# Kernel tuning notes

Hardware: AMD Instinct MI355X
Metric: run time of the kernel (lower is better)

## Reference

```python
import jax, jax.numpy as jnp
import numpy as np

DIM = 1024
DEPTH = 7
PAR = 8
N_NODES = 2 ** (DEPTH + 1) - 1  # 255
WIDTH = PAR * N_NODES  # 2040


def setup_inputs() -> dict:
    key = jax.random.key(0)
    k1, k2, k3, k4 = jax.random.split(key, 4)
    init_k = float(np.sqrt(1.0 / DIM))
    init_k2 = float(np.sqrt(1.0 / ((DEPTH + 1) * PAR)))
    oldx = jax.random.normal(k1, (4, 2048, DIM), dtype=jnp.float32)
    W_in = jax.random.uniform(k2, (WIDTH, DIM), jnp.float32, -init_k, init_k)
    b_in = jax.random.uniform(k3, (WIDTH,), jnp.float32, -init_k, init_k)
    W_out = jax.random.uniform(k4, (DIM, WIDTH), jnp.float32, -init_k2, init_k2)
    return {"oldx": oldx, "W_in": W_in, "b_in": b_in, "W_out": W_out}


def reference(oldx, W_in, b_in, W_out):
    x = oldx.reshape(-1, DIM)                      # [B, dim]
    B = x.shape[0]
    logits = x @ W_in.T + b_in                     # [B, width] dense GEMM over ALL nodes
    decisions = (logits > 0).astype(jnp.int32).reshape(B, PAR, N_NODES)
    acts = jax.nn.silu(logits).reshape(B, PAR, N_NODES)

    # Tree traversal: mark root, then descend DEPTH levels by each node's sign bit.
    current = jnp.zeros((B, PAR), dtype=jnp.int32)
    dmap = jax.nn.one_hot(current, N_NODES, dtype=acts.dtype)  # root node marked
    for d in range(DEPTH):
        cur_platform = 2 ** d - 1
        next_platform = 2 ** (d + 1) - 1
        moves = jnp.take_along_axis(decisions, current[..., None], axis=2)[..., 0]
        current = (current - cur_platform) * 2 + moves + next_platform
        dmap = dmap + jax.nn.one_hot(current, N_NODES, dtype=acts.dtype)

    masked = acts * jax.lax.stop_gradient(dmap)    # only depth+1 nodes per tree survive
    out = masked.reshape(B, WIDTH) @ W_out.T       # [B, dim]
    return out.reshape(oldx.shape)
```

## Files before the change

### kernel.cpp

```cpp
#include <hip/hip_runtime.h>
#include <math.h>

#define DIM 1024
#define DEPTH 7
#define PAR 8
#define N_NODES 255
#define WIDTH 2040
#define MARGIN 0.01f

#define REPLANE(p) ((((p) & 1) << 3) | ((((p) >> 1) & 1) << 4) | ((((p) >> 2) & 1) << 5))

typedef _Float16 half2v __attribute__((ext_vector_type(2)));

__device__ __forceinline__ half2v as_h2(unsigned int u) {
    union { unsigned int u; half2v h; } c; c.u = u; return c.h;
}
__device__ __forceinline__ unsigned int pack_h2(float a, float b) {
    union { half2v h; unsigned int u; } c;
    c.h = (half2v){(_Float16)a, (_Float16)b};
    return c.u;
}

__device__ __forceinline__ float dot2h(unsigned int a, unsigned int b, float c) {
#if __has_builtin(__builtin_amdgcn_fdot2)
    return __builtin_amdgcn_fdot2(as_h2(a), as_h2(b), c, false);
#else
    half2v ha = as_h2(a), hb = as_h2(b);
    c = fmaf((float)ha.x, (float)hb.x, c);
    return fmaf((float)ha.y, (float)hb.y, c);
#endif
}

__device__ __forceinline__ float foldK(float a, float b, int K) {
    const bool hi = (threadIdx.x & (unsigned)K) != 0;
    const float keep = hi ? b : a;
    const float send = hi ? a : b;
    return keep + __shfl_xor(send, K, 64);
}

#define PHASE_C_TREE(WLO, WHI, A) do {                                                      \
    const float a_ = (A); half2v h_;                                                        \
    h_ = as_h2((WLO).x); acc[0]  = fmaf((float)h_.x, a_, acc[0]);  acc[1]  = fmaf((float)h_.y, a_, acc[1]);  \
    h_ = as_h2((WLO).y); acc[2]  = fmaf((float)h_.x, a_, acc[2]);  acc[3]  = fmaf((float)h_.y, a_, acc[3]);  \
    h_ = as_h2((WLO).z); acc[4]  = fmaf((float)h_.x, a_, acc[4]);  acc[5]  = fmaf((float)h_.y, a_, acc[5]);  \
    h_ = as_h2((WLO).w); acc[6]  = fmaf((float)h_.x, a_, acc[6]);  acc[7]  = fmaf((float)h_.y, a_, acc[7]);  \
    h_ = as_h2((WHI).x); acc[8]  = fmaf((float)h_.x, a_, acc[8]);  acc[9]  = fmaf((float)h_.y, a_, acc[9]);  \
    h_ = as_h2((WHI).y); acc[10] = fmaf((float)h_.x, a_, acc[10]); acc[11] = fmaf((float)h_.y, a_, acc[11]); \
    h_ = as_h2((WHI).z); acc[12] = fmaf((float)h_.x, a_, acc[12]); acc[13] = fmaf((float)h_.y, a_, acc[13]); \
    h_ = as_h2((WHI).w); acc[14] = fmaf((float)h_.x, a_, acc[14]); acc[15] = fmaf((float)h_.y, a_, acc[15]); \
} while (0)

#define TRANS_BLOCKS 512

__global__ __launch_bounds__(256) void prep_kernel(
    const float* __restrict__ W_out,
    const float* __restrict__ W_in,
    unsigned short* __restrict__ WoT,
    unsigned int* __restrict__ Wh)
{
    __shared__ float tile[64][65];
    if (blockIdx.x < TRANS_BLOCKS) {
        const int w0 = (int)(blockIdx.x & 31) * 64;
        const int d0 = (int)(blockIdx.x >> 5) * 64;
        const int tid = (int)threadIdx.x;
        const int sub = tid & 15;
        const int grp = tid >> 4;

        #pragma unroll
        for (int pass = 0; pass < 4; ++pass) {
            const int dl = pass * 16 + grp;
            const int wl = sub * 4;
            const int w = w0 + wl;
            const int d = d0 + dl;
            float4 v = make_float4(0.f, 0.f, 0.f, 0.f);
            if (w + 3 < WIDTH) {
                v = *(const float4*)(W_out + (size_t)d * WIDTH + w);
            } else {
                float t0 = (w + 0 < WIDTH) ? W_out[(size_t)d * WIDTH + w + 0] : 0.f;
                float t1 = (w + 1 < WIDTH) ? W_out[(size_t)d * WIDTH + w + 1] : 0.f;
                float t2 = (w + 2 < WIDTH) ? W_out[(size_t)d * WIDTH + w + 2] : 0.f;
                float t3 = (w + 3 < WIDTH) ? W_out[(size_t)d * WIDTH + w + 3] : 0.f;
                v = make_float4(t0, t1, t2, t3);
            }
            tile[dl][wl + 0] = v.x; tile[dl][wl + 1] = v.y;
            tile[dl][wl + 2] = v.z; tile[dl][wl + 3] = v.w;
        }
        __syncthreads();
        #pragma unroll
        for (int pass = 0; pass < 4; ++pass) {
            const int wl = pass * 16 + grp;
            const int dl = sub * 4;
            const int w = w0 + wl;
            if (w < WIDTH) {
                uint2 pk;
                pk.x = pack_h2(tile[dl + 0][wl], tile[dl + 1][wl]);
                pk.y = pack_h2(tile[dl + 2][wl], tile[dl + 3][wl]);
                *(uint2*)(WoT + (size_t)w * DIM + d0 + dl) = pk;
            }
        }
    } else {
        const int n4 = WIDTH * DIM / 4;
        const int nthr = ((int)gridDim.x - TRANS_BLOCKS) * 256;
        for (int i = ((int)blockIdx.x - TRANS_BLOCKS) * 256 + (int)threadIdx.x;
             i < n4; i += nthr) {
            float4 v = ((const float4*)W_in)[i];
            uint2 pk;
            pk.x = pack_h2(v.x, v.y);
            pk.y = pack_h2(v.z, v.w);
            ((uint2*)Wh)[i] = pk;
        }
    }
}

__global__ __launch_bounds__(256) void fff_f16_kernel(
    const float* __restrict__ x,
    const float* __restrict__ W_in,
    const float* __restrict__ b_in,
    const unsigned int* __restrict__ Wh,
    const unsigned short* __restrict__ WoT,
    float* __restrict__ out,
    int B)
{
    const int wave = (int)((blockIdx.x * blockDim.x + threadIdx.x) >> 6);
    const int lane = (int)(threadIdx.x & 63);
    if (wave >= B) return;

    const float* xr = x + (size_t)wave * DIM;
    unsigned int xp[8];
    {
        float4 a0 = *(const float4*)(xr + lane * 8 + 0);
        float4 a1 = *(const float4*)(xr + lane * 8 + 4);
        float4 a2 = *(const float4*)(xr + 512 + lane * 8 + 0);
        float4 a3 = *(const float4*)(xr + 512 + lane * 8 + 4);
        xp[0] = pack_h2(a0.x, a0.y);
        xp[1] = pack_h2(a0.z, a0.w);
        xp[2] = pack_h2(a1.x, a1.y);
        xp[3] = pack_h2(a1.z, a1.w);
        xp[4] = pack_h2(a2.x, a2.y);
        xp[5] = pack_h2(a2.z, a2.w);
        xp[6] = pack_h2(a3.x, a3.y);
        xp[7] = pack_h2(a3.z, a3.w);
    }

    float acc[16];
    #pragma unroll
    for (int i = 0; i < 16; ++i) acc[i] = 0.f;

    unsigned long long nodes = 0ULL;
    const int myp = ((lane >> 3) & 1) | (((lane >> 4) & 1) << 1) | (((lane >> 5) & 1) << 2);

    #pragma unroll 1
    for (int d = 0; d <= DEPTH; ++d) {
        int gidx[PAR];
        #pragma unroll
        for (int p = 0; p < PAR; ++p) {
            const int np = (int)((nodes >> (8 * p)) & 0xffULL);
            gidx[p] = p * N_NODES + np;
        }

        const int ga = (lane & 8) ? gidx[1] : gidx[0];
        const int gb = (lane & 8) ? gidx[3] : gidx[2];
        const int gc = (lane & 8) ? gidx[5] : gidx[4];
        const int gd = (lane & 8) ? gidx[7] : gidx[6];
        const int ge = (lane & 16) ? gb : ga;
        const int gf = (lane & 16) ? gd : gc;
        const int gmine = (lane & 32) ? gf : ge;
        const float bias = b_in[gmine];

        uint4 ua[PAR], ub[PAR];
        #pragma unroll
        for (int p = 0; p < PAR; ++p) {
            const unsigned int* wr = Wh + (size_t)gidx[p] * (DIM / 2);
            ua[p] = *(const uint4*)(wr + lane * 4);
            ub[p] = *(const uint4*)(wr + 256 + lane * 4);
        }

        float partial[PAR];
        #pragma unroll
        for (int p = 0; p < PAR; ++p) {
            float s = 0.f;
            s = dot2h(xp[0], ua[p].x, s);
            s = dot2h(xp[1], ua[p].y, s);
            s = dot2h(xp[2], ua[p].z, s);
            s = dot2h(xp[3], ua[p].w, s);
            s = dot2h(xp[4], ub[p].x, s);
            s = dot2h(xp[5], ub[p].y, s);
            s = dot2h(xp[6], ub[p].z, s);
            s = dot2h(xp[7], ub[p].w, s);
            partial[p] = s;
        }

        uint4 wva[4], wvb[4];
        #pragma unroll
        for (int p = 0; p < 4; ++p) {
            const unsigned short* wo = WoT + (size_t)gidx[p] * DIM;
            wva[p] = *(const uint4*)(wo + lane * 8);
            wvb[p] = *(const uint4*)(wo + 512 + lane * 8);
        }

        const float c01 = foldK(partial[0], partial[1], 8);
        const float c23 = foldK(partial[2], partial[3], 8);
        const float c45 = foldK(partial[4], partial[5], 8);
        const float c67 = foldK(partial[6], partial[7], 8);
        const float d0f = foldK(c01, c23, 16);
        const float d1f = foldK(c45, c67, 16);
        float e = foldK(d0f, d1f, 32);
        e += __shfl_xor(e, 1, 64);
        e += __shfl_xor(e, 2, 64);
        e += __shfl_xor(e, 4, 64);
        float my = e + bias;

        if (d < DEPTH) {
            const unsigned long long bal = __ballot(fabsf(my) < MARGIN);
            unsigned rm = 0;
            #pragma unroll
            for (int p = 0; p < PAR; ++p)
                rm |= ((unsigned)((bal >> REPLANE(p)) & 1ULL)) << p;
            if (rm) {
                const float4 fa = *(const float4*)(xr + lane * 8 + 0);
                const float4 fb = *(const float4*)(xr + lane * 8 + 4);
                const float4 fc = *(const float4*)(xr + 512 + lane * 8 + 0);
                const float4 fd = *(const float4*)(xr + 512 + lane * 8 + 4);
                while (rm) {
                    const int p = __builtin_ctz(rm); rm &= (rm - 1u);
                    const int gi = gidx[p];
                    const float* wr = W_in + (size_t)gi * DIM;
                    const float4 wa = *(const float4*)(wr + lane * 8 + 0);
                    const float4 wb = *(const float4*)(wr + lane * 8 + 4);
                    const float4 wc = *(const float4*)(wr + 512 + lane * 8 + 0);
                    const float4 wd = *(const float4*)(wr + 512 + lane * 8 + 4);
                    float s = 0.f;
                    s = fmaf(fa.x, wa.x, s); s = fmaf(fa.y, wa.y, s);
                    s = fmaf(fa.z, wa.z, s); s = fmaf(fa.w, wa.w, s);
                    s = fmaf(fb.x, wb.x, s); s = fmaf(fb.y, wb.y, s);
                    s = fmaf(fb.z, wb.z, s); s = fmaf(fb.w, wb.w, s);
                    s = fmaf(fc.x, wc.x, s); s = fmaf(fc.y, wc.y, s);
                    s = fmaf(fc.z, wc.z, s); s = fmaf(fc.w, wc.w, s);
                    s = fmaf(fd.x, wd.x, s); s = fmaf(fd.y, wd.y, s);
                    s = fmaf(fd.z, wd.z, s); s = fmaf(fd.w, wd.w, s);
                    #pragma unroll
                    for (int off = 32; off >= 1; off >>= 1)
                        s += __shfl_xor(s, off, 64);
                    const float lf = s + b_in[gi];
                    my = (myp == p) ? lf : my;
                }
            }
        }

        const float act_mine = my / (1.0f + __expf(-my));
        const unsigned long long pos = __ballot(my > 0.0f);

        float act[PAR];
        #pragma unroll
        for (int p = 0; p < PAR; ++p)
            act[p] = __shfl(act_mine, REPLANE(p), 64);

        uint4 wvc[4], wvd[4];
        #pragma unroll
        for (int p = 0; p < 4; ++p) {
            const unsigned short* wo = WoT + (size_t)gidx[4 + p] * DIM;
            wvc[p] = *(const uint4*)(wo + lane * 8);
            wvd[p] = *(const uint4*)(wo + 512 + lane * 8);
        }

        #pragma unroll
        for (int p = 0; p < 4; ++p) PHASE_C_TREE(wva[p], wvb[p], act[p]);
        #pragma unroll
        for (int p = 0; p < 4; ++p) PHASE_C_TREE(wvc[p], wvd[p], act[4 + p]);

        if (d < DEPTH) {
            #pragma unroll
            for (int p = 0; p < PAR; ++p) {
                const int np = (int)((nodes >> (8 * p)) & 0xffULL);
                const unsigned long long nn = (unsigned long long)
                    (2 * np + 1 + (int)((pos >> REPLANE(p)) & 1ULL));
                nodes = (nodes & ~(0xffULL << (8 * p))) | (nn << (8 * p));
            }
        }
    }

    float* orow = out + (size_t)wave * DIM;
    *(float4*)(orow + lane * 8 + 0)       = make_float4(acc[0],  acc[1],  acc[2],  acc[3]);
    *(float4*)(orow + lane * 8 + 4)       = make_float4(acc[4],  acc[5],  acc[6],  acc[7]);
    *(float4*)(orow + 512 + lane * 8 + 0) = make_float4(acc[8],  acc[9],  acc[10], acc[11]);
    *(float4*)(orow + 512 + lane * 8 + 4) = make_float4(acc[12], acc[13], acc[14], acc[15]);
}

__global__ __launch_bounds__(256) void fff_fallback_kernel(
    const float* __restrict__ x, const float* __restrict__ W_in,
    const float* __restrict__ b_in, const float* __restrict__ W_out,
    float* __restrict__ out, int B)
{
    const int wave = (int)((blockIdx.x * blockDim.x + threadIdx.x) >> 6);
    const int lane = (int)(threadIdx.x & 63);
    if (wave >= B) return;

    const float* xr = x + (size_t)wave * DIM;
    float4 x4[4];
    x4[0] = *(const float4*)(xr + lane * 8 + 0);
    x4[1] = *(const float4*)(xr + lane * 8 + 4);
    x4[2] = *(const float4*)(xr + 512 + lane * 8 + 0);
    x4[3] = *(const float4*)(xr + 512 + lane * 8 + 4);

    float acc[16];
    #pragma unroll
    for (int i = 0; i < 16; ++i) acc[i] = 0.f;
    int node[PAR];
    #pragma unroll
    for (int p = 0; p < PAR; ++p) node[p] = 0;

    for (int d = 0; d <= DEPTH; ++d) {
        #pragma unroll
        for (int p = 0; p < PAR; ++p) {
            const int gidx = p * N_NODES + node[p];
            const float* wr = W_in + (size_t)gidx * DIM;
            const float4 wa = *(const float4*)(wr + lane * 8 + 0);
            const float4 wb = *(const float4*)(wr + lane * 8 + 4);
            const float4 wc = *(const float4*)(wr + 512 + lane * 8 + 0);
            const float4 wd = *(const float4*)(wr + 512 + lane * 8 + 4);
            float s = 0.f;
            s = fmaf(x4[0].x, wa.x, s); s = fmaf(x4[0].y, wa.y, s);
            s = fmaf(x4[0].z, wa.z, s); s = fmaf(x4[0].w, wa.w, s);
            s = fmaf(x4[1].x, wb.x, s); s = fmaf(x4[1].y, wb.y, s);
            s = fmaf(x4[1].z, wb.z, s); s = fmaf(x4[1].w, wb.w, s);
            s = fmaf(x4[2].x, wc.x, s); s = fmaf(x4[2].y, wc.y, s);
            s = fmaf(x4[2].z, wc.z, s); s = fmaf(x4[2].w, wc.w, s);
            s = fmaf(x4[3].x, wd.x, s); s = fmaf(x4[3].y, wd.y, s);
            s = fmaf(x4[3].z, wd.z, s); s = fmaf(x4[3].w, wd.w, s);
            #pragma unroll
            for (int off = 32; off >= 1; off >>= 1)
                s += __shfl_xor(s, off, 64);
            const float logit = s + b_in[gidx];
            const float act = logit / (1.0f + __expf(-logit));
            #pragma unroll
            for (int k = 0; k < 2; ++k) {
                #pragma unroll
                for (int j = 0; j < 8; ++j) {
                    const int e = k * 512 + lane * 8 + j;
                    acc[k * 8 + j] = fmaf(act, W_out[(size_t)e * WIDTH + gidx], acc[k * 8 + j]);
                }
            }
            node[p] = 2 * node[p] + 1 + ((logit > 0.0f) ? 1 : 0);
        }
    }

    float* orow = out + (size_t)wave * DIM;
    *(float4*)(orow + lane * 8 + 0)       = make_float4(acc[0],  acc[1],  acc[2],  acc[3]);
    *(float4*)(orow + lane * 8 + 4)       = make_float4(acc[4],  acc[5],  acc[6],  acc[7]);
    *(float4*)(orow + 512 + lane * 8 + 0) = make_float4(acc[8],  acc[9],  acc[10], acc[11]);
    *(float4*)(orow + 512 + lane * 8 + 4) = make_float4(acc[12], acc[13], acc[14], acc[15]);
}

extern "C" void kernel_launch(void* const* d_in, const int* in_sizes, int n_in,
                              void* d_out, int out_size, void* d_ws, size_t ws_size,
                              hipStream_t stream) {
    const float* oldx  = (const float*)d_in[0];
    const float* W_in  = (const float*)d_in[1];
    const float* b_in  = (const float*)d_in[2];
    const float* W_out = (const float*)d_in[3];
    float* out = (float*)d_out;

    const int B = in_sizes[0] / DIM;

    const size_t half = (size_t)WIDTH * DIM * sizeof(unsigned short);
    const bool use_lp = (ws_size >= 2 * half) && (d_ws != nullptr);

    const int blocks = (B + 3) / 4;

    if (use_lp) {
        unsigned short* WoT = (unsigned short*)d_ws;
        unsigned int*   Wh  = (unsigned int*)((char*)d_ws + half);
        prep_kernel<<<TRANS_BLOCKS + 1024, 256, 0, stream>>>(W_out, W_in, WoT, Wh);
        fff_f16_kernel<<<blocks, 256, 0, stream>>>(oldx, W_in, b_in, Wh, WoT, out, B);
    } else {
        fff_fallback_kernel<<<blocks, 256, 0, stream>>>(oldx, W_in, b_in, W_out, out, B);
    }
}
```

Before: 182.4 us.

## Drop load prefetching and raise occupancy via launch bounds to cut register pressure

Removes the early W_out prefetch (wva/wvb loaded before the reduction) and the batched W_in loads, replacing them with per-tree load-then-use loops. It also moves the bias load after the reduction and sets a minimum of 8 blocks per CU in __launch_bounds__. The aim is lower VGPR usage so more waves can hide memory latency. The cost is that the manual latency hiding inside each wave is lost, and W_out loads now sit on the critical path after the activation.

```diff
diff --git a/kernel.cpp b/kernel.cpp
--- a/kernel.cpp
+++ b/kernel.cpp
@@ -37,18 +37,6 @@
     const float send = hi ? a : b;
     return keep + __shfl_xor(send, K, 64);
 }
-
-#define PHASE_C_TREE(WLO, WHI, A) do {                                                      \
-    const float a_ = (A); half2v h_;                                                        \
-    h_ = as_h2((WLO).x); acc[0]  = fmaf((float)h_.x, a_, acc[0]);  acc[1]  = fmaf((float)h_.y, a_, acc[1]);  \
-    h_ = as_h2((WLO).y); acc[2]  = fmaf((float)h_.x, a_, acc[2]);  acc[3]  = fmaf((float)h_.y, a_, acc[3]);  \
-    h_ = as_h2((WLO).z); acc[4]  = fmaf((float)h_.x, a_, acc[4]);  acc[5]  = fmaf((float)h_.y, a_, acc[5]);  \
-    h_ = as_h2((WLO).w); acc[6]  = fmaf((float)h_.x, a_, acc[6]);  acc[7]  = fmaf((float)h_.y, a_, acc[7]);  \
-    h_ = as_h2((WHI).x); acc[8]  = fmaf((float)h_.x, a_, acc[8]);  acc[9]  = fmaf((float)h_.y, a_, acc[9]);  \
-    h_ = as_h2((WHI).y); acc[10] = fmaf((float)h_.x, a_, acc[10]); acc[11] = fmaf((float)h_.y, a_, acc[11]); \
-    h_ = as_h2((WHI).z); acc[12] = fmaf((float)h_.x, a_, acc[12]); acc[13] = fmaf((float)h_.y, a_, acc[13]); \
-    h_ = as_h2((WHI).w); acc[14] = fmaf((float)h_.x, a_, acc[14]); acc[15] = fmaf((float)h_.y, a_, acc[15]); \
-} while (0)
 
 #define TRANS_BLOCKS 512
 
@@ -112,7 +100,7 @@
     }
 }
 
-__global__ __launch_bounds__(256) void fff_f16_kernel(
+__global__ __launch_bounds__(256, 8) void fff_f16_kernel(
     const float* __restrict__ x,
     const float* __restrict__ W_in,
     const float* __restrict__ b_in,
@@ -158,44 +146,22 @@
             gidx[p] = p * N_NODES + np;
         }
 
-        const int ga = (lane & 8) ? gidx[1] : gidx[0];
-        const int gb = (lane & 8) ? gidx[3] : gidx[2];
-        const int gc = (lane & 8) ? gidx[5] : gidx[4];
-        const int gd = (lane & 8) ? gidx[7] : gidx[6];
-        const int ge = (lane & 16) ? gb : ga;
-        const int gf = (lane & 16) ? gd : gc;
-        const int gmine = (lane & 32) ? gf : ge;
-        const float bias = b_in[gmine];
-
-        uint4 ua[PAR], ub[PAR];
+        float partial[PAR];
         #pragma unroll
         for (int p = 0; p < PAR; ++p) {
             const unsigned int* wr = Wh + (size_t)gidx[p] * (DIM / 2);
-            ua[p] = *(const uint4*)(wr + lane * 4);
-            ub[p] = *(const uint4*)(wr + 256 + lane * 4);
-        }
-
-        float partial[PAR];
-        #pragma unroll
-        for (int p = 0; p < PAR; ++p) {
+            const uint4 u0 = *(const uint4*)(wr + lane * 4);
+            const uint4 u1 = *(const uint4*)(wr + 256 + lane * 4);
             float s = 0.f;
-            s = dot2h(xp[0], ua[p].x, s);
-            s = dot2h(xp[1], ua[p].y, s);
-            s = dot2h(xp[2], ua[p].z, s);
-            s = dot2h(xp[3], ua[p].w, s);
-            s = dot2h(xp[4], ub[p].x, s);
-            s = dot2h(xp[5], ub[p].y, s);
-            s = dot2h(xp[6], ub[p].z, s);
-            s = dot2h(xp[7], ub[p].w, s);
+            s = dot2h(xp[0], u0.x, s);
+            s = dot2h(xp[1], u0.y, s);
+            s = dot2h(xp[2], u0.z, s);
+            s = dot2h(xp[3], u0.w, s);
+            s = dot2h(xp[4], u1.x, s);
+            s = dot2h(xp[5], u1.y, s);
+            s = dot2h(xp[6], u1.z, s);
+            s = dot2h(xp[7], u1.w, s);
             partial[p] = s;
-        }
-
-        uint4 wva[4], wvb[4];
-        #pragma unroll
-        for (int p = 0; p < 4; ++p) {
-            const unsigned short* wo = WoT + (size_t)gidx[p] * DIM;
-            wva[p] = *(const uint4*)(wo + lane * 8);
-            wvb[p] = *(const uint4*)(wo + 512 + lane * 8);
         }
 
         const float c01 = foldK(partial[0], partial[1], 8);
@@ -208,7 +174,15 @@
         e += __shfl_xor(e, 1, 64);
         e += __shfl_xor(e, 2, 64);
         e += __shfl_xor(e, 4, 64);
-        float my = e + bias;
+
+        const int ga = (lane & 8) ? gidx[1] : gidx[0];
+        const int gb = (lane & 8) ? gidx[3] : gidx[2];
+        const int gc = (lane & 8) ? gidx[5] : gidx[4];
+        const int gd = (lane & 8) ? gidx[7] : gidx[6];
+        const int ge = (lane & 16) ? gb : ga;
+        const int gf = (lane & 16) ? gd : gc;
+        const int gmine = (lane & 32) ? gf : ge;
+        float my = e + b_in[gmine];
 
         if (d < DEPTH) {
             const unsigned long long bal = __ballot(fabsf(my) < MARGIN);
@@ -255,22 +229,23 @@
         for (int p = 0; p < PAR; ++p)
             act[p] = __shfl(act_mine, REPLANE(p), 64);
 
-        uint4 wvc[4], wvd[4];
-        #pragma unroll
-        for (int p = 0; p < 4; ++p) {
-            const unsigned short* wo = WoT + (size_t)gidx[4 + p] * DIM;
-            wvc[p] = *(const uint4*)(wo + lane * 8);
-            wvd[p] = *(const uint4*)(wo + 512 + lane * 8);
-        }
-
-        #pragma unroll
-        for (int p = 0; p < 4; ++p) PHASE_C_TREE(wva[p], wvb[p], act[p]);
-        #pragma unroll
-        for (int p = 0; p < 4; ++p) PHASE_C_TREE(wvc[p], wvd[p], act[4 + p]);
-
-        if (d < DEPTH) {
-            #pragma unroll
-            for (int p = 0; p < PAR; ++p) {
+        #pragma unroll
+        for (int p = 0; p < PAR; ++p) {
+            const unsigned short* wo = WoT + (size_t)gidx[p] * DIM;
+            const uint4 u0 = *(const uint4*)(wo + lane * 8);
+            const uint4 u1 = *(const uint4*)(wo + 512 + lane * 8);
+            const float a_ = act[p];
+            half2v h_;
+            h_ = as_h2(u0.x); acc[0]  = fmaf((float)h_.x, a_, acc[0]);  acc[1]  = fmaf((float)h_.y, a_, acc[1]);
+            h_ = as_h2(u0.y); acc[2]  = fmaf((float)h_.x, a_, acc[2]);  acc[3]  = fmaf((float)h_.y, a_, acc[3]);
+            h_ = as_h2(u0.z); acc[4]  = fmaf((float)h_.x, a_, acc[4]);  acc[5]  = fmaf((float)h_.y, a_, acc[5]);
+            h_ = as_h2(u0.w); acc[6]  = fmaf((float)h_.x, a_, acc[6]);  acc[7]  = fmaf((float)h_.y, a_, acc[7]);
+            h_ = as_h2(u1.x); acc[8]  = fmaf((float)h_.x, a_, acc[8]);  acc[9]  = fmaf((float)h_.y, a_, acc[9]);
+            h_ = as_h2(u1.y); acc[10] = fmaf((float)h_.x, a_, acc[10]); acc[11] = fmaf((float)h_.y, a_, acc[11]);
+            h_ = as_h2(u1.z); acc[12] = fmaf((float)h_.x, a_, acc[12]); acc[13] = fmaf((float)h_.y, a_, acc[13]);
+            h_ = as_h2(u1.w); acc[14] = fmaf((float)h_.x, a_, acc[14]); acc[15] = fmaf((float)h_.y, a_, acc[15]);
+
+            if (d < DEPTH) {
                 const int np = (int)((nodes >> (8 * p)) & 0xffULL);
                 const unsigned long long nn = (unsigned long long)
                     (2 * np + 1 + (int)((pos >> REPLANE(p)) & 1ULL));
```

After: 516.9 us. 2.83x slower.
